# Optimization experiments

Measured on AMD Instinct MI355X. Metric: run time of the kernel, lower is better.

## Reference

```python
import jax, jax.numpy as jnp
import numpy as np

N = 50000      # nodes
D = 128        # feature dim
NNZ = 800000   # edges (avg degree 16)
M = 30         # Chebyshev order

def setup_inputs() -> dict:
    key = jax.random.key(0)
    k1, k2, k3, k4, k5 = jax.random.split(key, 5)
    rows = jax.random.randint(k1, (NNZ,), 0, N)
    cols = jax.random.randint(k2, (NNZ,), 0, N)
    # scale so row sums (Gershgorin bound on spectral radius) stay ~< 1,
    # mimicking a rescaled Laplacian required for a stable Chebyshev recurrence
    vals = jax.random.uniform(k3, (NNZ,), dtype=jnp.float32) * (0.5 / 16.0)
    X = jax.random.normal(k4, (N, D), dtype=jnp.float32)
    coeffs = jax.random.normal(k5, (M,), dtype=jnp.float32)
    return {"rows": rows, "cols": cols, "vals": vals, "X": X, "coeffs": coeffs}

def _spmm(rows, cols, vals, X, n):
    # y[r] += vals[e] * X[c]  for each edge e=(r,c): sparse L @ X
    return jax.ops.segment_sum(vals[:, None] * X[cols], rows, num_segments=n)

def reference(rows, cols, vals, X, coeffs):
    n = X.shape[0]
    T0 = X                                   # T_0 = X
    T1 = _spmm(rows, cols, vals, X, n)       # T_1 = L @ X
    acc = coeffs[0] * T0 + coeffs[1] * T1
    def step(carry, ck):
        T0, T1, acc = carry
        Tk = 2.0 * _spmm(rows, cols, vals, T1, n) - T0   # T_k = 2 L T_{k-1} - T_{k-2}
        return (T1, Tk, acc + ck * Tk), None
    (_, _, acc), _ = jax.lax.scan(step, (T0, T1, acc), coeffs[2:])
    return acc
```

## Files before the change

kernel.cpp:

```cpp
#include <hip/hip_runtime.h>
#include <hip/hip_fp16.h>

#define FD 128
#define RPB 4


__global__ void zero_i32(int* __restrict__ p, int n) {
  int i = blockIdx.x * blockDim.x + threadIdx.x;
  if (i < n) p[i] = 0;
}

__global__ void hist_kernel(const int* __restrict__ rows, int* __restrict__ cnt, int nnz) {
  int i = blockIdx.x * blockDim.x + threadIdx.x;
  if (i < nnz) atomicAdd(&cnt[rows[i]], 1);
}

__global__ void block_reduce(const int* __restrict__ cnt, int* __restrict__ bsum, int n) {
  __shared__ int sm[256];
  int i = blockIdx.x * 256 + threadIdx.x;
  sm[threadIdx.x] = (i < n) ? cnt[i] : 0;
  __syncthreads();
  for (int off = 128; off > 0; off >>= 1) {
    if (threadIdx.x < off) sm[threadIdx.x] += sm[threadIdx.x + off];
    __syncthreads();
  }
  if (threadIdx.x == 0) bsum[blockIdx.x] = sm[0];
}

__global__ void scan_bsum(const int* __restrict__ bsum, int* __restrict__ bpre, int nb) {
  __shared__ int sm[1024];
  const int tid = threadIdx.x;
  sm[tid] = (tid < nb) ? bsum[tid] : 0;
  __syncthreads();
  for (int off = 1; off < 1024; off <<= 1) {
    int t = (tid >= off) ? sm[tid - off] : 0;
    __syncthreads();
    sm[tid] += t;
    __syncthreads();
  }
  if (tid < nb) bpre[tid] = (tid == 0) ? 0 : sm[tid - 1];
}

__global__ void block_scan(const int* __restrict__ cnt, const int* __restrict__ bpre,
                           int* __restrict__ row_ptr, int n) {
  __shared__ int sm[256];
  const int tid = threadIdx.x;
  int i = blockIdx.x * 256 + tid;
  sm[tid] = (i < n) ? cnt[i] : 0;
  __syncthreads();
  for (int off = 1; off < 256; off <<= 1) {
    int t = (tid >= off) ? sm[tid - off] : 0;
    __syncthreads();
    sm[tid] += t;
    __syncthreads();
  }
  if (i < n) row_ptr[i + 1] = sm[tid] + bpre[blockIdx.x];
  if (i == 0) row_ptr[0] = 0;
}

__global__ void copy_i32(const int* __restrict__ src, int* __restrict__ dst, int n) {
  int i = blockIdx.x * blockDim.x + threadIdx.x;
  if (i < n) dst[i] = src[i];
}

__global__ void scatter_kernel(const int* __restrict__ rows, const int* __restrict__ cols,
                               const float* __restrict__ vals, int* __restrict__ fill,
                               int2* __restrict__ pk, int nnz) {
  int i = blockIdx.x * blockDim.x + threadIdx.x;
  if (i < nnz) {
    int r = rows[i];
    int pos = atomicAdd(&fill[r], 1);
    pk[pos] = make_int2(cols[i], __float_as_int(vals[i]));
  }
}

__global__ void f32_to_f16(const float* __restrict__ src, __half* __restrict__ dst, int n4) {
  int i = blockIdx.x * blockDim.x + threadIdx.x;
  if (i < n4) {
    float4 v = ((const float4*)src)[i];
    __half2* d = (__half2*)dst + 2 * (size_t)i;
    d[0] = __floats2half2_rn(v.x, v.y);
    d[1] = __floats2half2_rn(v.z, v.w);
  }
}


__device__ __forceinline__ void fma_edge(const __half* __restrict__ T, int c, float v,
                                         int fl, float2 acc[4]) {
  uint4 raw = ((const uint4*)(T + (size_t)c * FD))[fl];
  const __half2* h = (const __half2*)&raw;
  float2 x0 = __half22float2(h[0]);
  float2 x1 = __half22float2(h[1]);
  float2 x2 = __half22float2(h[2]);
  float2 x3 = __half22float2(h[3]);
  acc[0].x = fmaf(v, x0.x, acc[0].x); acc[0].y = fmaf(v, x0.y, acc[0].y);
  acc[1].x = fmaf(v, x1.x, acc[1].x); acc[1].y = fmaf(v, x1.y, acc[1].y);
  acc[2].x = fmaf(v, x2.x, acc[2].x); acc[2].y = fmaf(v, x2.y, acc[2].y);
  acc[3].x = fmaf(v, x3.x, acc[3].x); acc[3].y = fmaf(v, x3.y, acc[3].y);
}

__device__ __forceinline__ void gather_row(const int* __restrict__ rp,
                                           const int2* __restrict__ pk,
                                           const __half* __restrict__ T,
                                           int r, int sub, int fl, float2 acc[4]) {
  int e = rp[r];
  const int end = rp[r + 1];
  for (; e + 8 <= end; e += 8) {
    int2 cv0 = pk[e + sub];
    int2 cv1 = pk[e + 4 + sub];
    fma_edge(T, cv0.x, __int_as_float(cv0.y), fl, acc);
    fma_edge(T, cv1.x, __int_as_float(cv1.y), fl, acc);
  }
  if (e + 4 <= end) {
    int2 cv = pk[e + sub];
    fma_edge(T, cv.x, __int_as_float(cv.y), fl, acc);
    e += 4;
  }
  if (e < end) {
    int idx = e + sub;
    int2 cv = pk[min(idx, end - 1)];
    float v = (idx < end) ? __int_as_float(cv.y) : 0.f;
    fma_edge(T, cv.x, v, fl, acc);
  }
}

__device__ __forceinline__ void reduce_subs(float2 acc[4]) {
#pragma unroll
  for (int m = 16; m < 64; m <<= 1) {
#pragma unroll
    for (int q = 0; q < 4; ++q) {
      acc[q].x += __shfl_xor(acc[q].x, m, 64);
      acc[q].y += __shfl_xor(acc[q].y, m, 64);
    }
  }
}


__global__ __launch_bounds__(256) void clen_step(
    const int* __restrict__ rp, const int2* __restrict__ pk,
    const __half* __restrict__ src, const __half* __restrict__ Xh, __half* pd,
    const float* __restrict__ coeffs, int k, int flags, int M, int n) {
  const int lane = threadIdx.x & 63;
  const int sub = lane >> 4, fl = lane & 15;
  const int r = blockIdx.x * RPB + (threadIdx.x >> 6);
  if (r >= n) return;
  float2 acc[4] = {{0.f,0.f},{0.f,0.f},{0.f,0.f},{0.f,0.f}};
  gather_row(rp, pk, src, r, sub, fl, acc);
  reduce_subs(acc);
  if (sub == 0) {
    float ck = coeffs[k];
    if (flags & 2) ck -= coeffs[M - 1];
    const float g2 = (flags & 4) ? 2.f * coeffs[M - 1] : 2.f;
    uint4 xr = ((const uint4*)(Xh + (size_t)r * FD))[fl];
    const __half2* xh = (const __half2*)&xr;
    float2 p[4] = {{0.f,0.f},{0.f,0.f},{0.f,0.f},{0.f,0.f}};
    if (flags & 1) {
      uint4 pr = ((const uint4*)(pd + (size_t)r * FD))[fl];
      const __half2* ph = (const __half2*)&pr;
#pragma unroll
      for (int q = 0; q < 4; ++q) p[q] = __half22float2(ph[q]);
    }
    uint4 orr;
    __half2* oh = (__half2*)&orr;
#pragma unroll
    for (int q = 0; q < 4; ++q) {
      float2 x = __half22float2(xh[q]);
      float tx = fmaf(g2, acc[q].x, fmaf(ck, x.x, -p[q].x));
      float ty = fmaf(g2, acc[q].y, fmaf(ck, x.y, -p[q].y));
      oh[q] = __floats2half2_rn(tx, ty);
    }
    ((uint4*)(pd + (size_t)r * FD))[fl] = orr;
  }
}

__global__ __launch_bounds__(256) void clen_final(
    const int* __restrict__ rp, const int2* __restrict__ pk,
    const __half* __restrict__ b1, const __half* __restrict__ b2,
    const float* __restrict__ X, float* __restrict__ out,
    const float* __restrict__ coeffs, int n) {
  const int lane = threadIdx.x & 63;
  const int sub = lane >> 4, fl = lane & 15;
  const int r = blockIdx.x * RPB + (threadIdx.x >> 6);
  if (r >= n) return;
  float2 acc[4] = {{0.f,0.f},{0.f,0.f},{0.f,0.f},{0.f,0.f}};
  gather_row(rp, pk, b1, r, sub, fl, acc);
  reduce_subs(acc);
  if (sub == 0) {
    const float c0 = coeffs[0];
    uint4 pr = ((const uint4*)(b2 + (size_t)r * FD))[fl];
    const __half2* ph = (const __half2*)&pr;
    float4 x0 = ((const float4*)(X + (size_t)r * FD))[fl * 2];
    float4 x1 = ((const float4*)(X + (size_t)r * FD))[fl * 2 + 1];
    float2 p0 = __half22float2(ph[0]), p1 = __half22float2(ph[1]);
    float2 p2 = __half22float2(ph[2]), p3 = __half22float2(ph[3]);
    float4 o0, o1;
    o0.x = fmaf(c0, x0.x, acc[0].x - p0.x);
    o0.y = fmaf(c0, x0.y, acc[0].y - p0.y);
    o0.z = fmaf(c0, x0.z, acc[1].x - p1.x);
    o0.w = fmaf(c0, x0.w, acc[1].y - p1.y);
    o1.x = fmaf(c0, x1.x, acc[2].x - p2.x);
    o1.y = fmaf(c0, x1.y, acc[2].y - p2.y);
    o1.z = fmaf(c0, x1.z, acc[3].x - p3.x);
    o1.w = fmaf(c0, x1.w, acc[3].y - p3.y);
    ((float4*)(out + (size_t)r * FD))[fl * 2] = o0;
    ((float4*)(out + (size_t)r * FD))[fl * 2 + 1] = o1;
  }
}


extern "C" void kernel_launch(void* const* d_in, const int* in_sizes, int n_in,
                              void* d_out, int out_size, void* d_ws, size_t ws_size,
                              hipStream_t stream) {
  const int* rows = (const int*)d_in[0];
  const int* cols = (const int*)d_in[1];
  const float* vals = (const float*)d_in[2];
  const float* X = (const float*)d_in[3];
  const float* coeffs = (const float*)d_in[4];
  float* out = (float*)d_out;

  const int nnz = in_sizes[0];
  const int n = in_sizes[3] / FD;
  const int M = in_sizes[4];

  auto align_up = [](size_t x) { return (x + 255) & ~(size_t)255; };
  char* w = (char*)d_ws;
  size_t off = 0;
  int* row_ptr = (int*)(w + off); off = align_up(off + (size_t)(n + 1) * 4);
  int* row_fill = (int*)(w + off); off = align_up(off + (size_t)n * 4);
  int* bsum = (int*)(w + off); off = align_up(off + 1024 * 4);
  int* bpre = (int*)(w + off); off = align_up(off + 1024 * 4);
  int2* pk = (int2*)(w + off); off = align_up(off + (size_t)nnz * 8);
  __half* Xh = (__half*)(w + off); off = align_up(off + (size_t)n * FD * 2);
  __half* buf0 = (__half*)(w + off); off = align_up(off + (size_t)n * FD * 2);
  __half* buf1 = (__half*)(w + off); off = align_up(off + (size_t)n * FD * 2);
  __half* bufs[2] = {buf0, buf1};
  (void)ws_size;

  const int B = 256;
  const int gN = (n + B - 1) / B;
  const int gE = (nnz + B - 1) / B;
  const int gS = (n + RPB - 1) / RPB;
  const int n4 = n * FD / 4;
  const int gC = (n4 + B - 1) / B;

  zero_i32<<<gN, B, 0, stream>>>(row_fill, n);
  hist_kernel<<<gE, B, 0, stream>>>(rows, row_fill, nnz);
  block_reduce<<<gN, B, 0, stream>>>(row_fill, bsum, n);
  scan_bsum<<<1, 1024, 0, stream>>>(bsum, bpre, gN);
  block_scan<<<gN, B, 0, stream>>>(row_fill, bpre, row_ptr, n);
  copy_i32<<<gN, B, 0, stream>>>(row_ptr, row_fill, n);
  scatter_kernel<<<gE, B, 0, stream>>>(rows, cols, vals, row_fill, pk, nnz);
  f32_to_f16<<<gC, B, 0, stream>>>(X, Xh, n4);

  clen_step<<<gS, B, 0, stream>>>(row_ptr, pk, Xh, Xh, bufs[(M - 2) & 1],
                                  coeffs, M - 2, 4, M, n);
  clen_step<<<gS, B, 0, stream>>>(row_ptr, pk, bufs[(M - 2) & 1], Xh, bufs[(M - 3) & 1],
                                  coeffs, M - 3, 2, M, n);
  for (int k = M - 4; k >= 1; --k) {
    clen_step<<<gS, B, 0, stream>>>(row_ptr, pk, bufs[(k + 1) & 1], Xh, bufs[k & 1],
                                    coeffs, k, 1, M, n);
  }
  clen_final<<<gS, B, 0, stream>>>(row_ptr, pk, bufs[1], bufs[0], X, out, coeffs, n);
}
```

Measured before the change: 1.146 ms.

## Split feature dimension into four 32-wide slices across interleaved blocks

Each row's SpMM gather is split into four 32-column slices, each handled by a separate block. The blocks are interleaved so that the slices of neighbouring rows run close together in time. Each wave now uses 8 sub-groups of 8 lanes, each lane loading 8 bytes, so more edges are in flight per wave. Index and element loads are marked nontemporal. The intent is more memory-level parallelism and better cache locality for the gathered half-precision rows. The cost is that every slice re-reads the CSR index and value stream, four times in total, and each gathered row access shrinks to 64 bytes.

Result: slower. 3.085 ms (+169.2%).

```diff
diff --git a/kernel.cpp b/kernel.cpp
--- a/kernel.cpp
+++ b/kernel.cpp
@@ -2,7 +2,10 @@
 #include <hip/hip_fp16.h>
 
 #define FD 128
+#define SW 32
+#define NSLICE 4
 #define RPB 4
+#define SUBS 8
 
 
 __global__ void zero_i32(int* __restrict__ p, int n) {
@@ -85,91 +88,118 @@
 }
 
 
-__device__ __forceinline__ void fma_edge(const __half* __restrict__ T, int c, float v,
-                                         int fl, float2 acc[4]) {
-  uint4 raw = ((const uint4*)(T + (size_t)c * FD))[fl];
+typedef int v2i __attribute__((ext_vector_type(2)));
+typedef unsigned int v2u __attribute__((ext_vector_type(2)));
+typedef float v4f __attribute__((ext_vector_type(4)));
+
+__device__ __forceinline__ int2 nt_ld_i2(const int2* p) {
+  v2i v = __builtin_nontemporal_load((const v2i*)p);
+  return make_int2(v.x, v.y);
+}
+__device__ __forceinline__ uint2 nt_ld_u2(const uint2* p) {
+  v2u v = __builtin_nontemporal_load((const v2u*)p);
+  return make_uint2(v.x, v.y);
+}
+__device__ __forceinline__ float4 nt_ld_f4(const float4* p) {
+  v4f v = __builtin_nontemporal_load((const v4f*)p);
+  return make_float4(v.x, v.y, v.z, v.w);
+}
+__device__ __forceinline__ void nt_st_f4(float4* p, float4 x) {
+  v4f v = {x.x, x.y, x.z, x.w};
+  __builtin_nontemporal_store(v, (v4f*)p);
+}
+
+
+__device__ __forceinline__ void fma_edge8(const __half* __restrict__ T, int c, float v,
+                                          int fl, float2 acc[2]) {
+  uint2 raw = ((const uint2*)(T + (size_t)c * FD))[fl];
   const __half2* h = (const __half2*)&raw;
   float2 x0 = __half22float2(h[0]);
   float2 x1 = __half22float2(h[1]);
-  float2 x2 = __half22float2(h[2]);
-  float2 x3 = __half22float2(h[3]);
   acc[0].x = fmaf(v, x0.x, acc[0].x); acc[0].y = fmaf(v, x0.y, acc[0].y);
   acc[1].x = fmaf(v, x1.x, acc[1].x); acc[1].y = fmaf(v, x1.y, acc[1].y);
-  acc[2].x = fmaf(v, x2.x, acc[2].x); acc[2].y = fmaf(v, x2.y, acc[2].y);
-  acc[3].x = fmaf(v, x3.x, acc[3].x); acc[3].y = fmaf(v, x3.y, acc[3].y);
 }
 
 __device__ __forceinline__ void gather_row(const int* __restrict__ rp,
                                            const int2* __restrict__ pk,
                                            const __half* __restrict__ T,
-                                           int r, int sub, int fl, float2 acc[4]) {
+                                           int r, int sub, int fl, float2 acc[2]) {
   int e = rp[r];
   const int end = rp[r + 1];
-  for (; e + 8 <= end; e += 8) {
-    int2 cv0 = pk[e + sub];
-    int2 cv1 = pk[e + 4 + sub];
-    fma_edge(T, cv0.x, __int_as_float(cv0.y), fl, acc);
-    fma_edge(T, cv1.x, __int_as_float(cv1.y), fl, acc);
-  }
-  if (e + 4 <= end) {
-    int2 cv = pk[e + sub];
-    fma_edge(T, cv.x, __int_as_float(cv.y), fl, acc);
-    e += 4;
+  for (; e + 16 <= end; e += 16) {
+    int2 cv0 = nt_ld_i2(pk + e + sub);
+    int2 cv1 = nt_ld_i2(pk + e + 8 + sub);
+    fma_edge8(T, cv0.x, __int_as_float(cv0.y), fl, acc);
+    fma_edge8(T, cv1.x, __int_as_float(cv1.y), fl, acc);
+  }
+  if (e + 8 <= end) {
+    int2 cv = nt_ld_i2(pk + e + sub);
+    fma_edge8(T, cv.x, __int_as_float(cv.y), fl, acc);
+    e += 8;
   }
   if (e < end) {
     int idx = e + sub;
-    int2 cv = pk[min(idx, end - 1)];
+    int2 cv = nt_ld_i2(pk + min(idx, end - 1));
     float v = (idx < end) ? __int_as_float(cv.y) : 0.f;
-    fma_edge(T, cv.x, v, fl, acc);
-  }
-}
-
-__device__ __forceinline__ void reduce_subs(float2 acc[4]) {
+    fma_edge8(T, cv.x, v, fl, acc);
+  }
+}
+
+__device__ __forceinline__ void reduce_subs(float2 acc[2]) {
 #pragma unroll
-  for (int m = 16; m < 64; m <<= 1) {
+  for (int m = 8; m < 64; m <<= 1) {
 #pragma unroll
-    for (int q = 0; q < 4; ++q) {
+    for (int q = 0; q < 2; ++q) {
       acc[q].x += __shfl_xor(acc[q].x, m, 64);
       acc[q].y += __shfl_xor(acc[q].y, m, 64);
     }
   }
 }
 
+__device__ __forceinline__ void decode_bid(int bid, int rbs, int& slice, int& rb) {
+  slice = (bid >> 1) & 3;
+  rb = ((bid >> 3) << 1) | (bid & 1);
+}
+
 
 __global__ __launch_bounds__(256) void clen_step(
     const int* __restrict__ rp, const int2* __restrict__ pk,
     const __half* __restrict__ src, const __half* __restrict__ Xh, __half* pd,
-    const float* __restrict__ coeffs, int k, int flags, int M, int n) {
+    const float* __restrict__ coeffs, int k, int flags, int M, int n, int rbs) {
+  int slice, rb;
+  decode_bid(blockIdx.x, rbs, slice, rb);
+  if (rb >= rbs) return;
   const int lane = threadIdx.x & 63;
-  const int sub = lane >> 4, fl = lane & 15;
-  const int r = blockIdx.x * RPB + (threadIdx.x >> 6);
+  const int sub = lane >> 3, fl = lane & 7;
+  const int r = rb * RPB + (threadIdx.x >> 6);
   if (r >= n) return;
-  float2 acc[4] = {{0.f,0.f},{0.f,0.f},{0.f,0.f},{0.f,0.f}};
-  gather_row(rp, pk, src, r, sub, fl, acc);
+  float2 acc[2] = {{0.f,0.f},{0.f,0.f}};
+  gather_row(rp, pk, src + slice * SW, r, sub, fl, acc);
   reduce_subs(acc);
   if (sub == 0) {
     float ck = coeffs[k];
     if (flags & 2) ck -= coeffs[M - 1];
     const float g2 = (flags & 4) ? 2.f * coeffs[M - 1] : 2.f;
-    uint4 xr = ((const uint4*)(Xh + (size_t)r * FD))[fl];
+    const size_t off = (size_t)r * FD + slice * SW;
+    uint2 xr = nt_ld_u2((const uint2*)(Xh + off) + fl);
     const __half2* xh = (const __half2*)&xr;
-    float2 p[4] = {{0.f,0.f},{0.f,0.f},{0.f,0.f},{0.f,0.f}};
+    float2 p[2] = {{0.f,0.f},{0.f,0.f}};
     if (flags & 1) {
-      uint4 pr = ((const uint4*)(pd + (size_t)r * FD))[fl];
+      uint2 pr = nt_ld_u2((const uint2*)(pd + off) + fl);
       const __half2* ph = (const __half2*)&pr;
-#pragma unroll
-      for (int q = 0; q < 4; ++q) p[q] = __half22float2(ph[q]);
+      p[0] = __half22float2(ph[0]);
+      p[1] = __half22float2(ph[1]);
     }
-    uint4 orr;
+    uint2 orr;
     __half2* oh = (__half2*)&orr;
 #pragma unroll
-    for (int q = 0; q < 4; ++q) {
+    for (int q = 0; q < 2; ++q) {
       float2 x = __half22float2(xh[q]);
       float tx = fmaf(g2, acc[q].x, fmaf(ck, x.x, -p[q].x));
       float ty = fmaf(g2, acc[q].y, fmaf(ck, x.y, -p[q].y));
       oh[q] = __floats2half2_rn(tx, ty);
     }
-    ((uint4*)(pd + (size_t)r * FD))[fl] = orr;
+    ((uint2*)(pd + off))[fl] = orr;
   }
 }
 
@@ -177,33 +207,30 @@
     const int* __restrict__ rp, const int2* __restrict__ pk,
     const __half* __restrict__ b1, const __half* __restrict__ b2,
     const float* __restrict__ X, float* __restrict__ out,
-    const float* __restrict__ coeffs, int n) {
+    const float* __restrict__ coeffs, int n, int rbs) {
+  int slice, rb;
+  decode_bid(blockIdx.x, rbs, slice, rb);
+  if (rb >= rbs) return;
   const int lane = threadIdx.x & 63;
-  const int sub = lane >> 4, fl = lane & 15;
-  const int r = blockIdx.x * RPB + (threadIdx.x >> 6);
+  const int sub = lane >> 3, fl = lane & 7;
+  const int r = rb * RPB + (threadIdx.x >> 6);
   if (r >= n) return;
-  float2 acc[4] = {{0.f,0.f},{0.f,0.f},{0.f,0.f},{0.f,0.f}};
-  gather_row(rp, pk, b1, r, sub, fl, acc);
+  float2 acc[2] = {{0.f,0.f},{0.f,0.f}};
+  gather_row(rp, pk, b1 + slice * SW, r, sub, fl, acc);
   reduce_subs(acc);
   if (sub == 0) {
     const float c0 = coeffs[0];
-    uint4 pr = ((const uint4*)(b2 + (size_t)r * FD))[fl];
+    const size_t off = (size_t)r * FD + slice * SW;
+    uint2 pr = nt_ld_u2((const uint2*)(b2 + off) + fl);
     const __half2* ph = (const __half2*)&pr;
-    float4 x0 = ((const float4*)(X + (size_t)r * FD))[fl * 2];
-    float4 x1 = ((const float4*)(X + (size_t)r * FD))[fl * 2 + 1];
     float2 p0 = __half22float2(ph[0]), p1 = __half22float2(ph[1]);
-    float2 p2 = __half22float2(ph[2]), p3 = __half22float2(ph[3]);
-    float4 o0, o1;
-    o0.x = fmaf(c0, x0.x, acc[0].x - p0.x);
-    o0.y = fmaf(c0, x0.y, acc[0].y - p0.y);
-    o0.z = fmaf(c0, x0.z, acc[1].x - p1.x);
-    o0.w = fmaf(c0, x0.w, acc[1].y - p1.y);
-    o1.x = fmaf(c0, x1.x, acc[2].x - p2.x);
-    o1.y = fmaf(c0, x1.y, acc[2].y - p2.y);
-    o1.z = fmaf(c0, x1.z, acc[3].x - p3.x);
-    o1.w = fmaf(c0, x1.w, acc[3].y - p3.y);
-    ((float4*)(out + (size_t)r * FD))[fl * 2] = o0;
-    ((float4*)(out + (size_t)r * FD))[fl * 2 + 1] = o1;
+    float4 x = nt_ld_f4((const float4*)(X + off) + fl);
+    float4 o;
+    o.x = fmaf(c0, x.x, acc[0].x - p0.x);
+    o.y = fmaf(c0, x.y, acc[0].y - p0.y);
+    o.z = fmaf(c0, x.z, acc[1].x - p1.x);
+    o.w = fmaf(c0, x.w, acc[1].y - p1.y);
+    nt_st_f4((float4*)(out + off) + fl, o);
   }
 }
 
@@ -239,7 +266,8 @@
   const int B = 256;
   const int gN = (n + B - 1) / B;
   const int gE = (nnz + B - 1) / B;
-  const int gS = (n + RPB - 1) / RPB;
+  const int rbs = (n + RPB - 1) / RPB;
+  const int gS = 8 * ((rbs + 1) / 2);
   const int n4 = n * FD / 4;
   const int gC = (n4 + B - 1) / B;
 
@@ -253,12 +281,12 @@
   f32_to_f16<<<gC, B, 0, stream>>>(X, Xh, n4);
 
   clen_step<<<gS, B, 0, stream>>>(row_ptr, pk, Xh, Xh, bufs[(M - 2) & 1],
-                                  coeffs, M - 2, 4, M, n);
+                                  coeffs, M - 2, 4, M, n, rbs);
   clen_step<<<gS, B, 0, stream>>>(row_ptr, pk, bufs[(M - 2) & 1], Xh, bufs[(M - 3) & 1],
-                                  coeffs, M - 3, 2, M, n);
+                                  coeffs, M - 3, 2, M, n, rbs);
   for (int k = M - 4; k >= 1; --k) {
     clen_step<<<gS, B, 0, stream>>>(row_ptr, pk, bufs[(k + 1) & 1], Xh, bufs[k & 1],
-                                    coeffs, k, 1, M, n);
-  }
-  clen_final<<<gS, B, 0, stream>>>(row_ptr, pk, bufs[1], bufs[0], X, out, coeffs, n);
-}
+                                    coeffs, k, 1, M, n, rbs);
+  }
+  clen_final<<<gS, B, 0, stream>>>(row_ptr, pk, bufs[1], bufs[0], X, out, coeffs, n, rbs);
+}
```

## Split feature dimension into two 64-wide slices with sliced half-precision layout

Applied to the files above, without the earlier changes.

Stores the fp16 feature buffers as two column slices of 64 halves each, laid out slice-major, and assigns each block to one slice. Block ids interleave slices so neighbouring blocks cover the same rows in different slices. Each wavefront now handles 8 edges at a time with 8 lanes per edge instead of 4 edges with 16 lanes. The aim is to shrink the per-slice gather working set (about 6.4 MB) so it stays cache-resident, at the cost of reading the CSR index data twice.

New measurement: 1.433 ms. 1.25x slower.

```diff
diff --git a/kernel.cpp b/kernel.cpp
--- a/kernel.cpp
+++ b/kernel.cpp
@@ -2,6 +2,7 @@
 #include <hip/hip_fp16.h>
 
 #define FD 128
+#define SW 64
 #define RPB 4
 
 
@@ -74,20 +75,25 @@
   }
 }
 
-__global__ void f32_to_f16(const float* __restrict__ src, __half* __restrict__ dst, int n4) {
+__global__ void f32_to_f16s(const float* __restrict__ src, __half* __restrict__ dst,
+                            int n, int n4) {
   int i = blockIdx.x * blockDim.x + threadIdx.x;
   if (i < n4) {
     float4 v = ((const float4*)src)[i];
-    __half2* d = (__half2*)dst + 2 * (size_t)i;
+    int r = i >> 5;
+    int d0 = (i & 31) * 4;
+    int s = d0 >> 6;
+    int o = d0 & 63;
+    __half2* d = (__half2*)(dst + (size_t)s * n * SW + (size_t)r * SW + o);
     d[0] = __floats2half2_rn(v.x, v.y);
     d[1] = __floats2half2_rn(v.z, v.w);
   }
 }
 
 
-__device__ __forceinline__ void fma_edge(const __half* __restrict__ T, int c, float v,
-                                         int fl, float2 acc[4]) {
-  uint4 raw = ((const uint4*)(T + (size_t)c * FD))[fl];
+__device__ __forceinline__ void fma_edge8(const __half* __restrict__ T, int c, float v,
+                                          int fl, float2 acc[4]) {
+  uint4 raw = ((const uint4*)(T + (size_t)c * SW))[fl];
   const __half2* h = (const __half2*)&raw;
   float2 x0 = __half22float2(h[0]);
   float2 x1 = __half22float2(h[1]);
@@ -105,28 +111,28 @@
                                            int r, int sub, int fl, float2 acc[4]) {
   int e = rp[r];
   const int end = rp[r + 1];
-  for (; e + 8 <= end; e += 8) {
+  for (; e + 16 <= end; e += 16) {
     int2 cv0 = pk[e + sub];
-    int2 cv1 = pk[e + 4 + sub];
-    fma_edge(T, cv0.x, __int_as_float(cv0.y), fl, acc);
-    fma_edge(T, cv1.x, __int_as_float(cv1.y), fl, acc);
-  }
-  if (e + 4 <= end) {
+    int2 cv1 = pk[e + 8 + sub];
+    fma_edge8(T, cv0.x, __int_as_float(cv0.y), fl, acc);
+    fma_edge8(T, cv1.x, __int_as_float(cv1.y), fl, acc);
+  }
+  if (e + 8 <= end) {
     int2 cv = pk[e + sub];
-    fma_edge(T, cv.x, __int_as_float(cv.y), fl, acc);
-    e += 4;
+    fma_edge8(T, cv.x, __int_as_float(cv.y), fl, acc);
+    e += 8;
   }
   if (e < end) {
     int idx = e + sub;
     int2 cv = pk[min(idx, end - 1)];
     float v = (idx < end) ? __int_as_float(cv.y) : 0.f;
-    fma_edge(T, cv.x, v, fl, acc);
+    fma_edge8(T, cv.x, v, fl, acc);
   }
 }
 
 __device__ __forceinline__ void reduce_subs(float2 acc[4]) {
 #pragma unroll
-  for (int m = 16; m < 64; m <<= 1) {
+  for (int m = 8; m < 64; m <<= 1) {
 #pragma unroll
     for (int q = 0; q < 4; ++q) {
       acc[q].x += __shfl_xor(acc[q].x, m, 64);
@@ -135,27 +141,38 @@
   }
 }
 
+__device__ __forceinline__ void decode_bid(int bid, int& slice, int& rb) {
+  const int x = bid & 7;
+  slice = x >> 2;
+  rb = ((bid >> 3) << 2) | (x & 3);
+}
+
 
 __global__ __launch_bounds__(256) void clen_step(
     const int* __restrict__ rp, const int2* __restrict__ pk,
     const __half* __restrict__ src, const __half* __restrict__ Xh, __half* pd,
-    const float* __restrict__ coeffs, int k, int flags, int M, int n) {
+    const float* __restrict__ coeffs, int k, int flags, int M, int n, int rbs) {
+  int slice, rb;
+  decode_bid(blockIdx.x, slice, rb);
+  if (rb >= rbs) return;
   const int lane = threadIdx.x & 63;
-  const int sub = lane >> 4, fl = lane & 15;
-  const int r = blockIdx.x * RPB + (threadIdx.x >> 6);
+  const int sub = lane >> 3, fl = lane & 7;
+  const int r = rb * RPB + (threadIdx.x >> 6);
   if (r >= n) return;
+  const size_t sp = (size_t)n * SW;
   float2 acc[4] = {{0.f,0.f},{0.f,0.f},{0.f,0.f},{0.f,0.f}};
-  gather_row(rp, pk, src, r, sub, fl, acc);
+  gather_row(rp, pk, src + slice * sp, r, sub, fl, acc);
   reduce_subs(acc);
   if (sub == 0) {
     float ck = coeffs[k];
     if (flags & 2) ck -= coeffs[M - 1];
     const float g2 = (flags & 4) ? 2.f * coeffs[M - 1] : 2.f;
-    uint4 xr = ((const uint4*)(Xh + (size_t)r * FD))[fl];
+    const size_t off = slice * sp + (size_t)r * SW;
+    uint4 xr = ((const uint4*)(Xh + off))[fl];
     const __half2* xh = (const __half2*)&xr;
     float2 p[4] = {{0.f,0.f},{0.f,0.f},{0.f,0.f},{0.f,0.f}};
     if (flags & 1) {
-      uint4 pr = ((const uint4*)(pd + (size_t)r * FD))[fl];
+      uint4 pr = ((const uint4*)(pd + off))[fl];
       const __half2* ph = (const __half2*)&pr;
 #pragma unroll
       for (int q = 0; q < 4; ++q) p[q] = __half22float2(ph[q]);
@@ -169,7 +186,7 @@
       float ty = fmaf(g2, acc[q].y, fmaf(ck, x.y, -p[q].y));
       oh[q] = __floats2half2_rn(tx, ty);
     }
-    ((uint4*)(pd + (size_t)r * FD))[fl] = orr;
+    ((uint4*)(pd + off))[fl] = orr;
   }
 }
 
@@ -177,20 +194,27 @@
     const int* __restrict__ rp, const int2* __restrict__ pk,
     const __half* __restrict__ b1, const __half* __restrict__ b2,
     const float* __restrict__ X, float* __restrict__ out,
-    const float* __restrict__ coeffs, int n) {
+    const float* __restrict__ coeffs, int n, int rbs) {
+  int slice, rb;
+  decode_bid(blockIdx.x, slice, rb);
+  if (rb >= rbs) return;
   const int lane = threadIdx.x & 63;
-  const int sub = lane >> 4, fl = lane & 15;
-  const int r = blockIdx.x * RPB + (threadIdx.x >> 6);
+  const int sub = lane >> 3, fl = lane & 7;
+  const int r = rb * RPB + (threadIdx.x >> 6);
   if (r >= n) return;
+  const size_t sp = (size_t)n * SW;
   float2 acc[4] = {{0.f,0.f},{0.f,0.f},{0.f,0.f},{0.f,0.f}};
-  gather_row(rp, pk, b1, r, sub, fl, acc);
+  gather_row(rp, pk, b1 + slice * sp, r, sub, fl, acc);
   reduce_subs(acc);
   if (sub == 0) {
     const float c0 = coeffs[0];
-    uint4 pr = ((const uint4*)(b2 + (size_t)r * FD))[fl];
+    const size_t off = slice * sp + (size_t)r * SW;
+    uint4 pr = ((const uint4*)(b2 + off))[fl];
     const __half2* ph = (const __half2*)&pr;
-    float4 x0 = ((const float4*)(X + (size_t)r * FD))[fl * 2];
-    float4 x1 = ((const float4*)(X + (size_t)r * FD))[fl * 2 + 1];
+    const float* Xs = X + (size_t)r * FD + slice * SW;
+    float* os = out + (size_t)r * FD + slice * SW;
+    float4 x0 = ((const float4*)Xs)[fl * 2];
+    float4 x1 = ((const float4*)Xs)[fl * 2 + 1];
     float2 p0 = __half22float2(ph[0]), p1 = __half22float2(ph[1]);
     float2 p2 = __half22float2(ph[2]), p3 = __half22float2(ph[3]);
     float4 o0, o1;
@@ -202,8 +226,8 @@
     o1.y = fmaf(c0, x1.y, acc[2].y - p2.y);
     o1.z = fmaf(c0, x1.z, acc[3].x - p3.x);
     o1.w = fmaf(c0, x1.w, acc[3].y - p3.y);
-    ((float4*)(out + (size_t)r * FD))[fl * 2] = o0;
-    ((float4*)(out + (size_t)r * FD))[fl * 2 + 1] = o1;
+    ((float4*)os)[fl * 2] = o0;
+    ((float4*)os)[fl * 2 + 1] = o1;
   }
 }
 
@@ -239,7 +263,8 @@
   const int B = 256;
   const int gN = (n + B - 1) / B;
   const int gE = (nnz + B - 1) / B;
-  const int gS = (n + RPB - 1) / RPB;
+  const int rbs = (n + RPB - 1) / RPB;
+  const int gS = 8 * ((rbs + 3) / 4);
   const int n4 = n * FD / 4;
   const int gC = (n4 + B - 1) / B;
 
@@ -250,15 +275,15 @@
   block_scan<<<gN, B, 0, stream>>>(row_fill, bpre, row_ptr, n);
   copy_i32<<<gN, B, 0, stream>>>(row_ptr, row_fill, n);
   scatter_kernel<<<gE, B, 0, stream>>>(rows, cols, vals, row_fill, pk, nnz);
-  f32_to_f16<<<gC, B, 0, stream>>>(X, Xh, n4);
+  f32_to_f16s<<<gC, B, 0, stream>>>(X, Xh, n, n4);
 
   clen_step<<<gS, B, 0, stream>>>(row_ptr, pk, Xh, Xh, bufs[(M - 2) & 1],
-                                  coeffs, M - 2, 4, M, n);
+                                  coeffs, M - 2, 4, M, n, rbs);
   clen_step<<<gS, B, 0, stream>>>(row_ptr, pk, bufs[(M - 2) & 1], Xh, bufs[(M - 3) & 1],
-                                  coeffs, M - 3, 2, M, n);
+                                  coeffs, M - 3, 2, M, n, rbs);
   for (int k = M - 4; k >= 1; --k) {
     clen_step<<<gS, B, 0, stream>>>(row_ptr, pk, bufs[(k + 1) & 1], Xh, bufs[k & 1],
-                                    coeffs, k, 1, M, n);
-  }
-  clen_final<<<gS, B, 0, stream>>>(row_ptr, pk, bufs[1], bufs[0], X, out, coeffs, n);
-}
+                                    coeffs, k, 1, M, n, rbs);
+  }
+  clen_final<<<gS, B, 0, stream>>>(row_ptr, pk, bufs[1], bufs[0], X, out, coeffs, n, rbs);
+}
```
